# Optimization experiments

Measured on AMD Instinct MI355X. Metric: run time of the kernel, lower is better.

Reference implementation:

```python
import jax, jax.numpy as jnp
import numpy as np

B, T, D, H = 8, 1024, 1024, 16
HD = D // H  # 64
FF = 4 * D


def setup_inputs() -> dict:
    key = jax.random.key(0)
    ks = jax.random.split(key, 16)
    s = lambda k, shape, scale: (jax.random.normal(k, shape, dtype=jnp.float32) * scale)
    return {
        "x": s(ks[0], (B, T, D), 1.0),
        "ln1_g": jnp.ones((D,), jnp.float32),
        "ln1_b": jnp.zeros((D,), jnp.float32),
        "ln2_g": jnp.ones((D,), jnp.float32),
        "ln2_b": jnp.zeros((D,), jnp.float32),
        "Wq": s(ks[1], (H, D, HD), 0.02), "bq": jnp.zeros((H, HD), jnp.float32),
        "Wk": s(ks[2], (H, D, HD), 0.02), "bk": jnp.zeros((H, HD), jnp.float32),
        "Wv": s(ks[3], (H, D, HD), 0.02), "bv": jnp.zeros((H, HD), jnp.float32),
        "Wo": s(ks[4], (D, D), 0.02), "bo": jnp.zeros((D,), jnp.float32),
        "W1": s(ks[5], (D, FF), 0.02), "b1": jnp.zeros((FF,), jnp.float32),
        "W2": s(ks[6], (FF, D), 0.02), "b2": jnp.zeros((D,), jnp.float32),
    }


def layer_norm(x, g, b, eps=1e-5):
    mu = jnp.mean(x, axis=-1, keepdims=True)
    var = jnp.mean(jnp.square(x - mu), axis=-1, keepdims=True)
    return (x - mu) * jax.lax.rsqrt(var + eps) * g + b


def reference(x, ln1_g, ln1_b, ln2_g, ln2_b, Wq, bq, Wk, bk, Wv, bv, Wo, bo, W1, b1, W2, b2):
    h = layer_norm(x, ln1_g, ln1_b)
    # Per-head Q/K/V projections, batched over heads (equivalent to the
    # Python loop of per-head Linears in the original module).
    q = jnp.einsum("btd,hde->bhte", h, Wq) + bq[None, :, None, :]
    k = jnp.einsum("btd,hde->bhte", h, Wk) + bk[None, :, None, :]
    v = jnp.einsum("btd,hde->bhte", h, Wv) + bv[None, :, None, :]
    scores = jnp.einsum("bhte,bhse->bhts", q, k) / jnp.sqrt(jnp.float32(HD))
    att = jax.nn.softmax(scores, axis=-1)  # no causal mask in source
    ctx = jnp.einsum("bhts,bhse->bhte", att, v)
    # concat heads along feature dim
    ctx = jnp.transpose(ctx, (0, 2, 1, 3)).reshape(B, T, D)
    attn_out = ctx @ Wo + bo
    x = x + attn_out
    h2 = layer_norm(x, ln2_g, ln2_b)
    ff = jax.nn.gelu(h2 @ W1 + b1, approximate=False) @ W2 + b2
    return x + ff
```

## Files before the change

kernel.cpp:

```cpp
#include <hip/hip_runtime.h>
#include <hip/hip_bf16.h>
#include <cstdint>
#include <cstddef>


typedef __bf16 bf16;
typedef __bf16 bf16x8 __attribute__((ext_vector_type(8)));
typedef __bf16 bf16x4 __attribute__((ext_vector_type(4)));
typedef float  f32x4  __attribute__((ext_vector_type(4)));
typedef uint32_t u32x4 __attribute__((ext_vector_type(4)));

#define BB    8
#define TT    1024
#define DD    1024
#define HH    16
#define HDIM  64
#define FFD   4096
#define MROWS (BB*TT)

__device__ __forceinline__ void async_ld16(const void* g, void* l) {
  __builtin_amdgcn_global_load_lds(
      (const __attribute__((address_space(1))) uint32_t*)g,
      (__attribute__((address_space(3))) uint32_t*)l, 16, 0, 0);
}

__device__ __forceinline__ float gelu_f(float v) {
  float z = 0.7978845608028654f * (v + 0.044715f * v * v * v);
  z = fminf(fmaxf(z, -9.0f), 9.0f);
  const float e = __expf(-2.0f * z);
  const float th = 1.0f - __fdividef(2.0f * e, 1.0f + e);
  return 0.5f * v * (1.0f + th);
}

__device__ __forceinline__ float exp2_fast(float x) {
  float r; asm("v_exp_f32 %0, %1" : "=v"(r) : "v"(x)); return r;
}
__device__ __forceinline__ uint32_t cvt_pk_bf16(float a, float b) {
  uint32_t r; asm("v_cvt_pk_bf16_f32 %0, %1, %2" : "=v"(r) : "v"(a), "v"(b));
  return r;
}

__global__ void k_transpose_cast(const float* __restrict__ src, bf16* __restrict__ dst,
                                 int K, int N) {
  __shared__ float tile[32][33];
  const size_t boff = (size_t)blockIdx.z * K * N;
  src += boff; dst += boff;
  const int k0 = blockIdx.y * 32, n0 = blockIdx.x * 32;
  const int tx = threadIdx.x, ty = threadIdx.y;
#pragma unroll
  for (int i = 0; i < 4; ++i)
    tile[ty + i*8][tx] = src[(size_t)(k0 + ty + i*8) * N + n0 + tx];
  __syncthreads();
#pragma unroll
  for (int i = 0; i < 4; ++i)
    dst[(size_t)(n0 + ty + i*8) * K + k0 + tx] = (bf16)tile[tx][ty + i*8];
}

__global__ void k_concat_bias(const float* __restrict__ bq, const float* __restrict__ bk,
                              const float* __restrict__ bv, float* __restrict__ out) {
  int i = blockIdx.x * 256 + threadIdx.x;
  float v = (i < 1024) ? bq[i] : (i < 2048) ? bk[i - 1024] : bv[i - 2048];
  out[i] = v;
}

__global__ void k_transpose_v(const bf16* __restrict__ qkv, bf16* __restrict__ vT) {
  __shared__ bf16 tile[32][33];
  const int bh = blockIdx.z;
  const int b = bh >> 4, h = bh & 15;
  const int t0 = blockIdx.x * 32, e0 = blockIdx.y * 32;
  const int tx = threadIdx.x, ty = threadIdx.y;
  const bf16* src = qkv + (size_t)b * TT * 3072 + 2048 + h * 64;
#pragma unroll
  for (int i = 0; i < 4; ++i)
    tile[ty + i*8][tx] = src[(size_t)(t0 + ty + i*8) * 3072 + e0 + tx];
  __syncthreads();
  bf16* dst = vT + ((size_t)bh * 64 + e0) * TT + t0;
#pragma unroll
  for (int i = 0; i < 4; ++i)
    dst[(size_t)(ty + i*8) * TT + tx] = tile[tx][ty + i*8];
}

__global__ void k_layernorm(const float* __restrict__ x, const float* __restrict__ g,
                            const float* __restrict__ b, bf16* __restrict__ out) {
  const int row = blockIdx.x, tid = threadIdx.x;
  const float* xr = x + (size_t)row * DD;
  f32x4 v = *(const f32x4*)(xr + tid * 4);
  float s  = v[0] + v[1] + v[2] + v[3];
  float ss = v[0]*v[0] + v[1]*v[1] + v[2]*v[2] + v[3]*v[3];
#pragma unroll
  for (int m = 1; m < 64; m <<= 1) { s += __shfl_xor(s, m); ss += __shfl_xor(ss, m); }
  __shared__ float red[8];
  const int wid = tid >> 6;
  if ((tid & 63) == 0) { red[wid*2] = s; red[wid*2+1] = ss; }
  __syncthreads();
  s  = red[0] + red[2] + red[4] + red[6];
  ss = red[1] + red[3] + red[5] + red[7];
  const float mu = s * (1.0f / DD);
  const float var = ss * (1.0f / DD) - mu * mu;
  const float rs = rsqrtf(var + 1e-5f);
  bf16x4 o;
#pragma unroll
  for (int j = 0; j < 4; ++j)
    o[j] = (bf16)((v[j] - mu) * rs * g[tid*4 + j] + b[tid*4 + j]);
  *(bf16x4*)&out[(size_t)row * DD + tid * 4] = o;
}

template<int MODE>
__global__ __launch_bounds__(256)
void k_gemm(const bf16* __restrict__ A, const bf16* __restrict__ Bt,
            const float* __restrict__ bias, const float* __restrict__ res,
            bf16* __restrict__ outb, float* __restrict__ outf,
            int M, int N, int K) {
  __shared__ __align__(16) bf16 As[128 * 64];
  __shared__ __align__(16) bf16 Bs[128 * 64];
  const int tid = threadIdx.x;
  const int w = tid >> 6, l = tid & 63;
  const int wm = w >> 1, wn = w & 1;
  const int l15 = l & 15, l4 = l >> 4;
  const int m0 = blockIdx.y * 128, n0 = blockIdx.x * 128;

  f32x4 acc[4][4] = {};

  const int l7 = l15 & 7;
  const int c0 = (l4 ^ l7) * 8, c1 = ((4 + l4) ^ l7) * 8;
  const bf16* const Ab = &As[(wm*64 + l15)*64];
  const bf16* const Bb = &Bs[(wn*64 + l15)*64];

  const int sr8 = l >> 3, sl7 = l & 7;
  const int schx = (sl7 ^ sr8) * 8;
  const bf16* const gA0 = A  + (size_t)(m0 + w*32 + sr8) * K + schx;
  const bf16* const gA1 = gA0 + (size_t)8 * K;
  const bf16* const gA2 = gA0 + (size_t)16 * K;
  const bf16* const gA3 = gA0 + (size_t)24 * K;
  const bf16* const gB0 = Bt + (size_t)(n0 + w*32 + sr8) * K + schx;
  const bf16* const gB1 = gB0 + (size_t)8 * K;
  const bf16* const gB2 = gB0 + (size_t)16 * K;
  const bf16* const gB3 = gB0 + (size_t)24 * K;
  bf16* const lA = (bf16*)As + w*32*64;
  bf16* const lB = (bf16*)Bs + w*32*64;

  for (int k0 = 0; k0 < K; k0 += 64) {
    async_ld16(gA0 + k0, lA);          async_ld16(gA1 + k0, lA + 8*64);
    async_ld16(gA2 + k0, lA + 16*64);  async_ld16(gA3 + k0, lA + 24*64);
    async_ld16(gB0 + k0, lB);          async_ld16(gB1 + k0, lB + 8*64);
    async_ld16(gB2 + k0, lB + 16*64);  async_ld16(gB3 + k0, lB + 24*64);
    __syncthreads();
#pragma unroll
    for (int kk = 0; kk < 2; ++kk) {
      const int cc = kk ? c1 : c0;
      bf16x8 af[4], bfr[4];
#pragma unroll
      for (int mf = 0; mf < 4; ++mf) af[mf] = *(const bf16x8*)(Ab + mf*1024 + cc);
#pragma unroll
      for (int nf = 0; nf < 4; ++nf) bfr[nf] = *(const bf16x8*)(Bb + nf*1024 + cc);
#pragma unroll
      for (int mf = 0; mf < 4; ++mf)
#pragma unroll
        for (int nf = 0; nf < 4; ++nf)
          acc[mf][nf] = __builtin_amdgcn_mfma_f32_16x16x32_bf16(af[mf], bfr[nf], acc[mf][nf], 0, 0, 0);
    }
    __syncthreads();
  }

#pragma unroll
  for (int mf = 0; mf < 4; ++mf) {
#pragma unroll
    for (int r = 0; r < 4; ++r) {
      const size_t grow = (size_t)(m0 + wm*64 + mf*16 + l4*4 + r);
      const size_t rowoff = grow * (size_t)N;
#pragma unroll
      for (int nf = 0; nf < 4; ++nf) {
        const int gcol = n0 + wn*64 + nf*16 + l15;
        float v = acc[mf][nf][r] + bias[gcol];
        if constexpr (MODE == 1) v = gelu_f(v);
        if constexpr (MODE == 2) {
          v += res[rowoff + gcol];
          outf[rowoff + gcol] = v;
        } else {
          outb[rowoff + gcol] = (bf16)v;
        }
      }
    }
  }
}

__global__ __launch_bounds__(512)
void k_attn(const bf16* __restrict__ qkv, const bf16* __restrict__ vT,
            bf16* __restrict__ ctx) {
  const int tid = threadIdx.x;
  const int w = tid >> 6, l = tid & 63;
  const int l15 = l & 15, l4 = l >> 4;

  const int gid = ((int)blockIdx.x & 7) * 128 + ((int)blockIdx.x >> 3);
  const int qt = gid & 7;
  const int bh = gid >> 3;
  const int h = bh & 15, b = bh >> 4;

  __shared__ __align__(16) bf16 Ks[2][64 * 64];
  __shared__ __align__(16) bf16 Vs[2][64 * 64];

  const bf16* base = qkv + (size_t)b * TT * 3072;
  const bf16* Qp = base + h * 64;
  const bf16* Kp = base + 1024 + h * 64;
  const bf16* Vtp = vT + (size_t)bh * HDIM * TT;

  const float SCL = 0.125f * 1.44269504f;
  const float THR = 8.0f * 1.44269504f;

  const int qrow = qt * 128 + w * 16 + l15;
  bf16x8 qf[2];
  {
    bf16x8 q0 = *(const bf16x8*)&Qp[(size_t)qrow * 3072 + l4 * 8];
    bf16x8 q1 = *(const bf16x8*)&Qp[(size_t)qrow * 3072 + 32 + l4 * 8];
#pragma unroll
    for (int j = 0; j < 8; ++j) {
      qf[0][j] = (bf16)((float)q0[j] * SCL);
      qf[1][j] = (bf16)((float)q1[j] * SCL);
    }
  }

  f32x4 oacc[4] = {};
  float mrow = -1e30f;
  float lrow = 0.f;

  const int l7 = l15 & 7;
  const int c0 = (l4 ^ l7) * 8, c1 = ((4 + l4) ^ l7) * 8;

  const int aL0 = (((l4 & 1) << 5) + l15) << 2;
  const int aL1 = aL0 + 64;
  const bool hi = (l & 32) != 0;

  const int srow = w * 8 + (l >> 3);
  const int sch = (l & 7) ^ (srow & 7);

  auto stage = [&](int buf, int t) {
    const int kv0 = t * 64;
    async_ld16(Kp + (size_t)(kv0 + srow) * 3072 + sch * 8, &Ks[buf][w * 512]);
    async_ld16(Vtp + (size_t)srow * TT + kv0 + sch * 8, &Vs[buf][w * 512]);
  };

  stage(0, 0);
  for (int t = 0; t < TT / 64; ++t) {
    const int cur = t & 1;
    __syncthreads();
    if (t + 1 < TT / 64) stage(cur ^ 1, t + 1);

    const bf16* const Kc = &Ks[cur][l15 * 64];
    const bf16* const Vc = &Vs[cur][l15 * 64];

    f32x4 sacc[4] = {};
    __builtin_amdgcn_s_setprio(1);
#pragma unroll
    for (int nf = 0; nf < 4; ++nf) {
      bf16x8 k0 = *(const bf16x8*)(Kc + nf*1024 + c0);
      bf16x8 k1 = *(const bf16x8*)(Kc + nf*1024 + c1);
      sacc[nf] = __builtin_amdgcn_mfma_f32_16x16x32_bf16(k0, qf[0], sacc[nf], 0, 0, 0);
      sacc[nf] = __builtin_amdgcn_mfma_f32_16x16x32_bf16(k1, qf[1], sacc[nf], 0, 0, 0);
    }
    __builtin_amdgcn_s_setprio(0);

    float m = fmaxf(fmaxf(sacc[0][0], sacc[0][1]), fmaxf(sacc[0][2], sacc[0][3]));
#pragma unroll
    for (int nf = 1; nf < 4; ++nf)
      m = fmaxf(m, fmaxf(fmaxf(sacc[nf][0], sacc[nf][1]), fmaxf(sacc[nf][2], sacc[nf][3])));
    m = fmaxf(m, __shfl_xor(m, 16));
    m = fmaxf(m, __shfl_xor(m, 32));

    const int ok = (m <= mrow + THR);
    if (!__all(ok)) {
      const float mn = fmaxf(mrow, m);
      const float e = exp2_fast(mrow - mn);
      mrow = mn;
      lrow *= e;
      const int qb = l4 << 2;
      float e0 = __shfl(e, qb + 0), e1 = __shfl(e, qb + 1);
      float e2 = __shfl(e, qb + 2), e3 = __shfl(e, qb + 3);
#pragma unroll
      for (int nf = 0; nf < 4; ++nf) {
        oacc[nf][0] *= e0; oacc[nf][1] *= e1;
        oacc[nf][2] *= e2; oacc[nf][3] *= e3;
      }
    }

    float p[4][4];
    float ls = 0.f;
    uint32_t pk0[4], pk1[4];
#pragma unroll
    for (int nf = 0; nf < 4; ++nf) {
#pragma unroll
      for (int r = 0; r < 4; ++r) {
        p[nf][r] = exp2_fast(sacc[nf][r] - mrow);
        ls += p[nf][r];
      }
      pk0[nf] = cvt_pk_bf16(p[nf][0], p[nf][1]);
      pk1[nf] = cvt_pk_bf16(p[nf][2], p[nf][3]);
    }
    ls += __shfl_xor(ls, 16);
    ls += __shfl_xor(ls, 32);
    lrow += ls;

    __builtin_amdgcn_s_setprio(1);
#pragma unroll
    for (int kk = 0; kk < 2; ++kk) {
      const int nfa = 2*kk, nfb = 2*kk + 1;
      int u0 = __builtin_amdgcn_ds_bpermute(aL0, (int)pk0[nfa]);
      int u1 = __builtin_amdgcn_ds_bpermute(aL0, (int)pk0[nfb]);
      int v0 = __builtin_amdgcn_ds_bpermute(aL0, (int)pk1[nfa]);
      int v1 = __builtin_amdgcn_ds_bpermute(aL0, (int)pk1[nfb]);
      int x0 = __builtin_amdgcn_ds_bpermute(aL1, (int)pk0[nfa]);
      int x1 = __builtin_amdgcn_ds_bpermute(aL1, (int)pk0[nfb]);
      int y0 = __builtin_amdgcn_ds_bpermute(aL1, (int)pk1[nfa]);
      int y1 = __builtin_amdgcn_ds_bpermute(aL1, (int)pk1[nfb]);
      u32x4 pw;
      pw[0] = (uint32_t)(hi ? u1 : u0);
      pw[1] = (uint32_t)(hi ? v1 : v0);
      pw[2] = (uint32_t)(hi ? x1 : x0);
      pw[3] = (uint32_t)(hi ? y1 : y0);
      bf16x8 pa = __builtin_bit_cast(bf16x8, pw);
      const int cc = kk ? c1 : c0;
#pragma unroll
      for (int nf = 0; nf < 4; ++nf) {
        bf16x8 vb = *(const bf16x8*)(Vc + nf*1024 + cc);
        oacc[nf] = __builtin_amdgcn_mfma_f32_16x16x32_bf16(pa, vb, oacc[nf], 0, 0, 0);
      }
    }
    __builtin_amdgcn_s_setprio(0);
  }

  const int qb = l4 << 2;
  float li0 = 1.0f / __shfl(lrow, qb + 0);
  float li1 = 1.0f / __shfl(lrow, qb + 1);
  float li2 = 1.0f / __shfl(lrow, qb + 2);
  float li3 = 1.0f / __shfl(lrow, qb + 3);
  bf16* outp = ctx + ((size_t)b * TT + qt * 128 + w * 16) * DD + h * 64;
#pragma unroll
  for (int nf = 0; nf < 4; ++nf) {
    outp[(size_t)(qb + 0) * DD + l15 + nf*16] = (bf16)(oacc[nf][0] * li0);
    outp[(size_t)(qb + 1) * DD + l15 + nf*16] = (bf16)(oacc[nf][1] * li1);
    outp[(size_t)(qb + 2) * DD + l15 + nf*16] = (bf16)(oacc[nf][2] * li2);
    outp[(size_t)(qb + 3) * DD + l15 + nf*16] = (bf16)(oacc[nf][3] * li3);
  }
}

extern "C" void kernel_launch(void* const* d_in, const int* in_sizes, int n_in,
                              void* d_out, int out_size, void* d_ws, size_t ws_size,
                              hipStream_t stream) {
  const float* x     = (const float*)d_in[0];
  const float* ln1_g = (const float*)d_in[1];
  const float* ln1_b = (const float*)d_in[2];
  const float* ln2_g = (const float*)d_in[3];
  const float* ln2_b = (const float*)d_in[4];
  const float* Wq    = (const float*)d_in[5];
  const float* bq    = (const float*)d_in[6];
  const float* Wk    = (const float*)d_in[7];
  const float* bk    = (const float*)d_in[8];
  const float* Wv    = (const float*)d_in[9];
  const float* bv    = (const float*)d_in[10];
  const float* Wo    = (const float*)d_in[11];
  const float* bo    = (const float*)d_in[12];
  const float* W1    = (const float*)d_in[13];
  const float* b1    = (const float*)d_in[14];
  const float* W2    = (const float*)d_in[15];
  const float* b2    = (const float*)d_in[16];
  float* out = (float*)d_out;

  char* ws = (char*)d_ws;
  bf16* h1    = (bf16*)(ws + 0);
  bf16* vT    = (bf16*)(ws + 0);
  bf16* qkv   = (bf16*)(ws + 16777216);
  bf16* ctx   = (bf16*)(ws + 67108864);
  bf16* u     = (bf16*)(ws + 16777216);
  float* x1   = (float*)(ws + 83886080);
  bf16* wtqkv = (bf16*)(ws + 117440512);
  bf16* wot   = (bf16*)(ws + 123731968);
  bf16* w1t   = (bf16*)(ws + 125829120);
  bf16* w2t   = (bf16*)(ws + 134217728);
  float* bqkv = (float*)(ws + 142606336);
  bf16* h2 = h1;

  dim3 tb(32, 8);
  k_transpose_cast<<<dim3(2, 32, 16), tb, 0, stream>>>(Wq, wtqkv, DD, HDIM);
  k_transpose_cast<<<dim3(2, 32, 16), tb, 0, stream>>>(Wk, wtqkv + 1024*1024, DD, HDIM);
  k_transpose_cast<<<dim3(2, 32, 16), tb, 0, stream>>>(Wv, wtqkv + 2048*1024, DD, HDIM);
  k_transpose_cast<<<dim3(32, 32, 1), tb, 0, stream>>>(Wo, wot, DD, DD);
  k_transpose_cast<<<dim3(128, 32, 1), tb, 0, stream>>>(W1, w1t, DD, FFD);
  k_transpose_cast<<<dim3(32, 128, 1), tb, 0, stream>>>(W2, w2t, FFD, DD);
  k_concat_bias<<<dim3(12), 256, 0, stream>>>(bq, bk, bv, bqkv);

  k_layernorm<<<dim3(MROWS), 256, 0, stream>>>(x, ln1_g, ln1_b, h1);

  k_gemm<0><<<dim3(24, 64), 256, 0, stream>>>(h1, wtqkv, bqkv, nullptr,
                                              qkv, nullptr, MROWS, 3072, DD);

  k_transpose_v<<<dim3(32, 2, 128), tb, 0, stream>>>(qkv, vT);

  k_attn<<<dim3(1024), 512, 0, stream>>>(qkv, vT, ctx);

  k_gemm<2><<<dim3(8, 64), 256, 0, stream>>>(ctx, wot, bo, x,
                                             nullptr, x1, MROWS, DD, DD);

  k_layernorm<<<dim3(MROWS), 256, 0, stream>>>(x1, ln2_g, ln2_b, h2);

  k_gemm<1><<<dim3(32, 64), 256, 0, stream>>>(h2, w1t, b1, nullptr,
                                              u, nullptr, MROWS, FFD, DD);

  k_gemm<2><<<dim3(8, 64), 256, 0, stream>>>(u, w2t, b2, x1,
                                             nullptr, out, MROWS, DD, FFD);

  (void)in_sizes; (void)n_in; (void)out_size; (void)ws_size;
}
```

Before: 435.1 us.

## Add 256x256 double-buffered GEMM kernels for QKV and FFN1 projections

Adds two new 512-thread GEMM kernels that use 256x256 output tiles with double-buffered LDS, XOR-swizzled async global-to-LDS loads, interleaved MFMA phases with s_setprio, and an XCD-aware block swizzle. They replace the 128x128 GEMM for the QKV projection and the first FFN matmul. The larger tiles raise arithmetic intensity and overlap loads with compute. In exchange they use more LDS and registers, which lowers occupancy, and the hand-placed waitcnt and barrier schedule adds correctness risk.

```diff
diff --git a/kernel.cpp b/kernel.cpp
--- a/kernel.cpp
+++ b/kernel.cpp
@@ -103,6 +103,201 @@
   for (int j = 0; j < 4; ++j)
     o[j] = (bf16)((v[j] - mu) * rs * g[tid*4 + j] + b[tid*4 + j]);
   *(bf16x4*)&out[(size_t)row * DD + tid * 4] = o;
+}
+
+#define RD_B(reg, base) { _Pragma("unroll") \
+    for (int nf = 0; nf < 4; ++nf) reg[nf] = *(const bf16x8*)((base) + nf*1024); }
+#define RD_A4(reg, base, mb) { _Pragma("unroll") \
+    for (int mf = 0; mf < 4; ++mf) reg[mf] = *(const bf16x8*)((base) + (mb+mf)*1024); }
+#define MM(areg, breg, mb) { _Pragma("unroll") \
+    for (int mf = 0; mf < 4; ++mf) _Pragma("unroll") \
+      for (int nf = 0; nf < 4; ++nf) \
+        acc[mb+mf][nf] = __builtin_amdgcn_mfma_f32_16x16x32_bf16(areg[mf], breg[nf], acc[mb+mf][nf], 0, 0, 0); }
+#define SGA(off, lb) { async_ld16(aG0 + (off), (lb)+0*64);   async_ld16(aG1 + (off), (lb)+64*64); \
+                       async_ld16(aG2 + (off), (lb)+128*64); async_ld16(aG3 + (off), (lb)+192*64); }
+#define SGB(off, lb) { async_ld16(bG0 + (off), (lb)+0*64);   async_ld16(bG1 + (off), (lb)+64*64); \
+                       async_ld16(bG2 + (off), (lb)+128*64); async_ld16(bG3 + (off), (lb)+192*64); }
+#define SGB2a(off, lb) { async_ld16(bG0 + (off), (lb)+0*64);   async_ld16(bG1 + (off), (lb)+64*64); }
+#define SGB2b(off, lb) { async_ld16(bG2 + (off), (lb)+128*64); async_ld16(bG3 + (off), (lb)+192*64); }
+#define WAIT_LGKM { asm volatile("s_waitcnt lgkmcnt(0)" ::: "memory"); __builtin_amdgcn_sched_barrier(0); }
+#define VMC(n)  { asm volatile("s_waitcnt vmcnt(" #n ")" ::: "memory"); __builtin_amdgcn_sched_barrier(0); }
+#define BAR __builtin_amdgcn_s_barrier()
+#define PR1 __builtin_amdgcn_s_setprio(1)
+#define PR0 __builtin_amdgcn_s_setprio(0)
+
+#define GEMM256_PREAMBLE \
+  __shared__ __align__(16) bf16 As[2][256 * 64]; \
+  __shared__ __align__(16) bf16 Bs[2][256 * 64]; \
+  const int tid = threadIdx.x; \
+  const int w = tid >> 6, l = tid & 63; \
+  const int wm = w >> 2, wn = w & 3; \
+  const int l15 = l & 15, l4 = l >> 4; \
+  const int nbx = N >> 8; \
+  const int nwg = gridDim.x; \
+  const int cpx = nwg >> 3; \
+  const int swz = (blockIdx.x & 7) * cpx + (blockIdx.x >> 3); \
+  const int m0 = (swz / nbx) << 8, n0 = (swz % nbx) << 8; \
+  f32x4 acc[8][4] = {}; \
+  const int l7 = l15 & 7; \
+  const int c0 = (l4 ^ l7) * 8; \
+  const int c1 = ((4 + l4) ^ l7) * 8; \
+  const bf16* const A00 = &As[0][(wm*128 + l15)*64 + c0]; \
+  const bf16* const A01 = &As[0][(wm*128 + l15)*64 + c1]; \
+  const bf16* const A10 = &As[1][(wm*128 + l15)*64 + c0]; \
+  const bf16* const A11 = &As[1][(wm*128 + l15)*64 + c1]; \
+  const bf16* const B00 = &Bs[0][(wn*64 + l15)*64 + c0]; \
+  const bf16* const B01 = &Bs[0][(wn*64 + l15)*64 + c1]; \
+  const bf16* const B10 = &Bs[1][(wn*64 + l15)*64 + c0]; \
+  const bf16* const B11 = &Bs[1][(wn*64 + l15)*64 + c1]; \
+  const int srow = l >> 3, sch = l & 7; \
+  const int schx = (sch ^ srow) * 8; \
+  const bf16* const aG0 = A  + (size_t)(m0 + w*8 + srow) * K + schx; \
+  const bf16* const aG1 = aG0 + (size_t)64 * K; \
+  const bf16* const aG2 = aG0 + (size_t)128 * K; \
+  const bf16* const aG3 = aG0 + (size_t)192 * K; \
+  const bf16* const bG0 = Bt + (size_t)(n0 + w*8 + srow) * K + schx; \
+  const bf16* const bG1 = bG0 + (size_t)64 * K; \
+  const bf16* const bG2 = bG0 + (size_t)128 * K; \
+  const bf16* const bG3 = bG0 + (size_t)192 * K; \
+  bf16* const LA0 = (bf16*)As[0] + w*512; \
+  bf16* const LA1 = (bf16*)As[1] + w*512; \
+  bf16* const LB0 = (bf16*)Bs[0] + w*512; \
+  bf16* const LB1 = (bf16*)Bs[1] + w*512; \
+  const int NT = K >> 6;
+
+#define GEMM256_EPILOGUE \
+  _Pragma("unroll") \
+  for (int mf = 0; mf < 8; ++mf) { \
+    _Pragma("unroll") \
+    for (int r = 0; r < 4; ++r) { \
+      const size_t grow = (size_t)(m0 + wm*128 + mf*16 + l4*4 + r); \
+      const size_t rowoff = grow * (size_t)N; \
+      _Pragma("unroll") \
+      for (int nf = 0; nf < 4; ++nf) { \
+        const int gcol = n0 + wn*64 + nf*16 + l15; \
+        float v = acc[mf][nf][r] + bias[gcol]; \
+        if constexpr (MODE == 1) v = gelu_f(v); \
+        outb[rowoff + gcol] = (bf16)v; \
+      } \
+    } \
+  }
+
+template<int MODE>
+__global__ __launch_bounds__(512, 2)
+void k_gemm256(const bf16* __restrict__ A, const bf16* __restrict__ Bt,
+               const float* __restrict__ bias, bf16* __restrict__ outb,
+               int M, int N, int K) {
+  GEMM256_PREAMBLE
+
+  SGA(0, LA0)  SGB2a(0, LB0) SGB2b(0, LB0)  SGA(64, LA1)
+  VMC(4);
+  BAR;
+
+  size_t ko = 0;
+  for (int T = 0; T < NT; T += 2) {
+    const bool nl  = (T + 2 < NT);
+    const bool nl2 = (T + 3 < NT);
+    bf16x8 b0[4], b1[4], alo[4], ahi[4];
+
+    RD_B(b0, B00) RD_A4(alo, A00, 0)
+    SGB2a(ko + 64, LB1)
+    BAR; WAIT_LGKM;
+    PR1; MM(alo, b0, 0) PR0;
+    BAR;
+    RD_A4(ahi, A00, 4)
+    SGB2b(ko + 64, LB1)
+    BAR; WAIT_LGKM;
+    PR1; MM(ahi, b0, 4) PR0;
+    BAR;
+    RD_B(b1, B01) RD_A4(alo, A01, 0) RD_A4(ahi, A01, 4)
+    BAR; WAIT_LGKM;
+    PR1; MM(alo, b1, 0) PR0;
+    BAR;
+    if (nl) SGA(ko + 128, LA0)
+    PR1; MM(ahi, b1, 4) PR0;
+    if (nl) { VMC(4); } else { VMC(0); }
+    BAR;
+
+    RD_B(b0, B10) RD_A4(alo, A10, 0)
+    if (nl) SGB2a(ko + 128, LB0)
+    BAR; WAIT_LGKM;
+    PR1; MM(alo, b0, 0) PR0;
+    BAR;
+    RD_A4(ahi, A10, 4)
+    if (nl) SGB2b(ko + 128, LB0)
+    BAR; WAIT_LGKM;
+    PR1; MM(ahi, b0, 4) PR0;
+    BAR;
+    RD_B(b1, B11) RD_A4(alo, A11, 0) RD_A4(ahi, A11, 4)
+    BAR; WAIT_LGKM;
+    PR1; MM(alo, b1, 0) PR0;
+    BAR;
+    if (nl2) SGA(ko + 192, LA1)
+    PR1; MM(ahi, b1, 4) PR0;
+    if (nl2) { VMC(4); } else { VMC(0); }
+    BAR;
+
+    ko += 128;
+  }
+
+  GEMM256_EPILOGUE
+}
+
+template<int MODE>
+__global__ __launch_bounds__(512, 2)
+void k_gemm256b(const bf16* __restrict__ A, const bf16* __restrict__ Bt,
+                const float* __restrict__ bias, bf16* __restrict__ outb,
+                int M, int N, int K) {
+  GEMM256_PREAMBLE
+
+  SGA(0, LA0)  SGB(0, LB0)  SGA(64, LA1)  SGB(64, LB1)
+  VMC(8);
+  BAR;
+
+  size_t ko = 0;
+  for (int T = 0; T < NT; T += 2) {
+    const bool nl  = (T + 2 < NT);
+    const bool nl2 = (T + 3 < NT);
+    bf16x8 b0[4], b1[4], alo[4], ahi[4];
+
+    RD_B(b0, B00) RD_A4(alo, A00, 0)
+    BAR; WAIT_LGKM;
+    PR1; MM(alo, b0, 0) PR0;
+    BAR;
+    RD_A4(ahi, A00, 4)
+    BAR; WAIT_LGKM;
+    PR1; MM(ahi, b0, 4) PR0;
+    BAR;
+    RD_B(b1, B01) RD_A4(alo, A01, 0) RD_A4(ahi, A01, 4)
+    BAR; WAIT_LGKM;
+    PR1; MM(alo, b1, 0) PR0;
+    BAR;
+    if (nl) { SGA(ko + 128, LA0) SGB(ko + 128, LB0) }
+    PR1; MM(ahi, b1, 4) PR0;
+    if (nl) { VMC(8); } else { VMC(0); }
+    BAR;
+
+    RD_B(b0, B10) RD_A4(alo, A10, 0)
+    BAR; WAIT_LGKM;
+    PR1; MM(alo, b0, 0) PR0;
+    BAR;
+    RD_A4(ahi, A10, 4)
+    BAR; WAIT_LGKM;
+    PR1; MM(ahi, b0, 4) PR0;
+    BAR;
+    RD_B(b1, B11) RD_A4(alo, A11, 0) RD_A4(ahi, A11, 4)
+    BAR; WAIT_LGKM;
+    PR1; MM(alo, b1, 0) PR0;
+    BAR;
+    if (nl2) { SGA(ko + 192, LA1) SGB(ko + 192, LB1) }
+    PR1; MM(ahi, b1, 4) PR0;
+    if (nl2) { VMC(8); } else { VMC(0); }
+    BAR;
+
+    ko += 128;
+  }
+
+  GEMM256_EPILOGUE
 }
 
 template<int MODE>
@@ -389,8 +584,8 @@
 
   k_layernorm<<<dim3(MROWS), 256, 0, stream>>>(x, ln1_g, ln1_b, h1);
 
-  k_gemm<0><<<dim3(24, 64), 256, 0, stream>>>(h1, wtqkv, bqkv, nullptr,
-                                              qkv, nullptr, MROWS, 3072, DD);
+  k_gemm256<0><<<dim3((MROWS/256)*(3072/256)), 512, 0, stream>>>(
+      h1, wtqkv, bqkv, qkv, MROWS, 3072, DD);
 
   k_transpose_v<<<dim3(32, 2, 128), tb, 0, stream>>>(qkv, vT);
 
@@ -401,8 +596,8 @@
 
   k_layernorm<<<dim3(MROWS), 256, 0, stream>>>(x1, ln2_g, ln2_b, h2);
 
-  k_gemm<1><<<dim3(32, 64), 256, 0, stream>>>(h2, w1t, b1, nullptr,
-                                              u, nullptr, MROWS, FFD, DD);
+  k_gemm256b<1><<<dim3((MROWS/256)*(FFD/256)), 512, 0, stream>>>(
+      h2, w1t, b1, u, MROWS, FFD, DD);
 
   k_gemm<2><<<dim3(8, 64), 256, 0, stream>>>(u, w2t, b2, x1,
                                              nullptr, out, MROWS, DD, FFD);
```

Measured after the change: 413.7 us. 1.05x faster.
